# Optimization experiments

Measured on AMD Instinct MI355X. Metric: run time of the kernel, lower is better.

## Reference

```python
import jax, jax.numpy as jnp
import numpy as np

B, K_MAIN, D = 2048, 511, 64


def setup_inputs() -> dict:
    key = jax.random.key(0)
    ks = jax.random.split(key, 8)
    return {
        "vals": jax.random.uniform(ks[0], (B, K_MAIN, D), dtype=jnp.float32),
        "log_density": jax.random.normal(ks[1], (K_MAIN, D), dtype=jnp.float32),
        "logits": jax.random.normal(ks[2], (K_MAIN, D), dtype=jnp.float32),
        "beta_raw": jax.random.normal(ks[3], (K_MAIN,), dtype=jnp.float32),
        "null_vals": jax.random.uniform(ks[4], (B,), dtype=jnp.float32),
        "null_log_density": jax.random.normal(ks[5], (D,), dtype=jnp.float32),
        "null_logits": jax.random.normal(ks[6], (D,), dtype=jnp.float32),
        "null_beta_raw": jax.random.normal(ks[7], (1,), dtype=jnp.float32),
    }


def reference(vals, log_density, logits, beta_raw, null_vals,
              null_log_density, null_logits, null_beta_raw):
    # MenuElement.weights = softmax(logits) per element; beta = clamp(softplus, 0, 10)
    weights = jax.nn.softmax(logits, axis=1)                      # (K_main, D)
    betas = jnp.clip(jax.nn.softplus(beta_raw), 0.0, 10.0)        # (K_main,)
    ld = jnp.clip(log_density, -10.0, 0.0)                        # (K_main, D)
    log_weights = jnp.log(weights + 1e-10) + ld                   # (K_main, D)
    M = jnp.max(log_weights, axis=1, keepdims=True)               # (K_main, 1)
    w_exp = jnp.exp(log_weights - M)                              # (K_main, D)
    # weighted reduction over D for every (valuation b, menu element k)
    weighted_sum = jnp.einsum('bkd,kd->bk', vals, w_exp)          # (B, K_main)
    u_main = jnp.exp(M[:, 0])[None, :] * weighted_sum - betas[None, :]

    # null element
    null_w = jax.nn.softmax(null_logits, axis=0)                  # (D,)
    null_ld = jnp.clip(null_log_density, -10.0, 0.0)
    log_weight_null = jnp.log(null_w + 1e-10) + null_ld           # (D,)
    null_beta = jnp.clip(jax.nn.softplus(null_beta_raw), 0.0, 10.0)[0]
    u_null = jnp.exp(log_weight_null[0]) * null_vals - null_beta  # (B,)

    U = jnp.concatenate([u_main, u_null[:, None]], axis=1)        # (B, K)
    return U
```

## Files before the change

### kernel.cpp

```cpp
#include <hip/hip_runtime.h>
#include <hip/hip_bf16.h>
#include <math.h>

#define B_SZ   2048
#define K_MAIN 511
#define K_OUT  512
#define D_SZ   64

#define WS_COEF  0
#define WS_BETAS (K_MAIN * D_SZ)

typedef float f4v __attribute__((ext_vector_type(4)));

__device__ __forceinline__ float softplus_clip(float x) {
    float sp = (x > 20.f) ? x : log1pf(expf(x));
    return fminf(fmaxf(sp, 0.f), 10.f);
}

__global__ void precompute_kernel(const float* __restrict__ log_density,
                                  const float* __restrict__ logits,
                                  const float* __restrict__ beta_raw,
                                  const float* __restrict__ null_log_density,
                                  const float* __restrict__ null_logits,
                                  const float* __restrict__ null_beta_raw,
                                  const float* __restrict__ null_vals,
                                  float* __restrict__ ws,
                                  float* __restrict__ out) {
    const int k    = blockIdx.x;
    const int lane = threadIdx.x;

    {
        float lg = logits[k * D_SZ + lane];
        float m = lg;
        #pragma unroll
        for (int off = 1; off < 64; off <<= 1) m = fmaxf(m, __shfl_xor(m, off));
        float e = expf(lg - m);
        float s = e;
        #pragma unroll
        for (int off = 1; off < 64; off <<= 1) s += __shfl_xor(s, off);
        float w = e / s;
        float ld = fminf(fmaxf(log_density[k * D_SZ + lane], -10.f), 0.f);
        ws[WS_COEF + k * D_SZ + lane] = (w + 1e-10f) * expf(ld);
        if (lane == 0) {
            ws[WS_BETAS + k] = softplus_clip(beta_raw[k]);
        }
    }

    if (k < (B_SZ / 64)) {
        float lg = null_logits[lane];
        float m = lg;
        #pragma unroll
        for (int off = 1; off < 64; off <<= 1) m = fmaxf(m, __shfl_xor(m, off));
        float e = expf(lg - m);
        float s = e;
        #pragma unroll
        for (int off = 1; off < 64; off <<= 1) s += __shfl_xor(s, off);
        float w0 = expf(null_logits[0] - m) / s;
        float ld0 = fminf(fmaxf(null_log_density[0], -10.f), 0.f);
        float c_null = (w0 + 1e-10f) * expf(ld0);
        float nbeta  = softplus_clip(null_beta_raw[0]);
        const int b = k * 64 + lane;
        out[(size_t)b * K_OUT + K_MAIN] = c_null * null_vals[b] - nbeta;
    }
}

__global__ void __launch_bounds__(256)
main_kernel(const float* __restrict__ vals,
            const float* __restrict__ ws,
            float* __restrict__ out) {
    const float* __restrict__ coef  = ws + WS_COEF;
    const float* __restrict__ betas = ws + WS_BETAS;

    const unsigned tid     = blockIdx.x * blockDim.x + threadIdx.x;
    const unsigned lane    = threadIdx.x & 63u;
    const unsigned wave    = tid >> 6;
    const unsigned nwaves  = (gridDim.x * blockDim.x) >> 6;
    const unsigned sub     = lane >> 4;
    const unsigned d0      = (lane & 15u) << 2;

    const unsigned total_rows = B_SZ * K_MAIN;
    const unsigned nquads     = total_rows >> 4;

    for (unsigned q = wave; q < nquads; q += nwaves) {
        const unsigned r0 = (q << 4) + sub;

        const f4v v0 = *reinterpret_cast<const f4v*>(vals + (size_t)r0 * D_SZ + d0);
        const f4v v1 = *reinterpret_cast<const f4v*>(vals + (size_t)(r0 + 4) * D_SZ + d0);
        const f4v v2 = *reinterpret_cast<const f4v*>(vals + (size_t)(r0 + 8) * D_SZ + d0);
        const f4v v3 = *reinterpret_cast<const f4v*>(vals + (size_t)(r0 + 12) * D_SZ + d0);

        unsigned k0 = r0 % K_MAIN;
        unsigned b0 = r0 / K_MAIN;
        unsigned k1 = k0 + 4, b1 = b0; if (k1 >= K_MAIN) { k1 -= K_MAIN; ++b1; }
        unsigned k2 = k1 + 4, b2 = b1; if (k2 >= K_MAIN) { k2 -= K_MAIN; ++b2; }
        unsigned k3 = k2 + 4, b3 = b2; if (k3 >= K_MAIN) { k3 -= K_MAIN; ++b3; }

        const f4v c0 = *reinterpret_cast<const f4v*>(coef + (size_t)k0 * D_SZ + d0);
        const f4v c1 = *reinterpret_cast<const f4v*>(coef + (size_t)k1 * D_SZ + d0);
        const f4v c2 = *reinterpret_cast<const f4v*>(coef + (size_t)k2 * D_SZ + d0);
        const f4v c3 = *reinterpret_cast<const f4v*>(coef + (size_t)k3 * D_SZ + d0);

        float p0 = v0.x * c0.x + v0.y * c0.y + v0.z * c0.z + v0.w * c0.w;
        float p1 = v1.x * c1.x + v1.y * c1.y + v1.z * c1.z + v1.w * c1.w;
        float p2 = v2.x * c2.x + v2.y * c2.y + v2.z * c2.z + v2.w * c2.w;
        float p3 = v3.x * c3.x + v3.y * c3.y + v3.z * c3.z + v3.w * c3.w;

        p0 += __shfl_xor(p0, 1);  p1 += __shfl_xor(p1, 1);
        p2 += __shfl_xor(p2, 1);  p3 += __shfl_xor(p3, 1);
        p0 += __shfl_xor(p0, 2);  p1 += __shfl_xor(p1, 2);
        p2 += __shfl_xor(p2, 2);  p3 += __shfl_xor(p3, 2);
        p0 += __shfl_xor(p0, 4);  p1 += __shfl_xor(p1, 4);
        p2 += __shfl_xor(p2, 4);  p3 += __shfl_xor(p3, 4);
        p0 += __shfl_xor(p0, 8);  p1 += __shfl_xor(p1, 8);
        p2 += __shfl_xor(p2, 8);  p3 += __shfl_xor(p3, 8);

        if ((lane & 15u) == 0u) {
            out[(size_t)b0 * K_OUT + k0] = p0 - betas[k0];
            out[(size_t)b1 * K_OUT + k1] = p1 - betas[k1];
            out[(size_t)b2 * K_OUT + k2] = p2 - betas[k2];
            out[(size_t)b3 * K_OUT + k3] = p3 - betas[k3];
        }
    }
}

extern "C" void kernel_launch(void* const* d_in, const int* in_sizes, int n_in,
                              void* d_out, int out_size, void* d_ws, size_t ws_size,
                              hipStream_t stream) {
    const float* vals             = (const float*)d_in[0];
    const float* log_density      = (const float*)d_in[1];
    const float* logits           = (const float*)d_in[2];
    const float* beta_raw         = (const float*)d_in[3];
    const float* null_vals        = (const float*)d_in[4];
    const float* null_log_density = (const float*)d_in[5];
    const float* null_logits      = (const float*)d_in[6];
    const float* null_beta_raw    = (const float*)d_in[7];

    float* out = (float*)d_out;
    float* ws  = (float*)d_ws;

    precompute_kernel<<<K_MAIN, 64, 0, stream>>>(log_density, logits, beta_raw,
                                                 null_log_density, null_logits,
                                                 null_beta_raw, null_vals, ws, out);

    main_kernel<<<4096, 256, 0, stream>>>(vals, ws, out);
}
```

Baseline: 48.90 us.

## Fuse precompute and main kernels into one cooperative launch with grid sync

Merges the coefficient/beta precompute kernel and the main dot-product kernel into a single cooperative kernel. Waves first compute coefficients and the null column, then a grid-wide barrier separates that phase from the persistent streaming reduction over vals. This removes one kernel launch and the inter-kernel gap. In exchange it adds a grid sync, caps the grid at 1024 blocks so they can be co-resident, and adds a launch_bounds occupancy hint.

After: 121.1 us. +147.7%, slower.

```diff
diff --git a/kernel.cpp b/kernel.cpp
--- a/kernel.cpp
+++ b/kernel.cpp
@@ -1,6 +1,8 @@
 #include <hip/hip_runtime.h>
-#include <hip/hip_bf16.h>
+#include <hip/hip_cooperative_groups.h>
 #include <math.h>
+
+namespace cg = cooperative_groups;
 
 #define B_SZ   2048
 #define K_MAIN 511
@@ -10,6 +12,8 @@
 #define WS_COEF  0
 #define WS_BETAS (K_MAIN * D_SZ)
 
+#define GRID_BLOCKS 1024
+
 typedef float f4v __attribute__((ext_vector_type(4)));
 
 __device__ __forceinline__ float softplus_clip(float x) {
@@ -17,19 +21,23 @@
     return fminf(fmaxf(sp, 0.f), 10.f);
 }
 
-__global__ void precompute_kernel(const float* __restrict__ log_density,
-                                  const float* __restrict__ logits,
-                                  const float* __restrict__ beta_raw,
-                                  const float* __restrict__ null_log_density,
-                                  const float* __restrict__ null_logits,
-                                  const float* __restrict__ null_beta_raw,
-                                  const float* __restrict__ null_vals,
-                                  float* __restrict__ ws,
-                                  float* __restrict__ out) {
-    const int k    = blockIdx.x;
-    const int lane = threadIdx.x;
+__global__ void __launch_bounds__(256, 4)
+fused_kernel(const float* __restrict__ vals,
+             const float* __restrict__ log_density,
+             const float* __restrict__ logits,
+             const float* __restrict__ beta_raw,
+             const float* __restrict__ null_vals,
+             const float* __restrict__ null_log_density,
+             const float* __restrict__ null_logits,
+             const float* __restrict__ null_beta_raw,
+             float* __restrict__ ws,
+             float* __restrict__ out) {
+    const unsigned tid   = blockIdx.x * blockDim.x + threadIdx.x;
+    const unsigned lane  = threadIdx.x & 63u;
+    const unsigned gwave = tid >> 6;
 
-    {
+    if (gwave < K_MAIN) {
+        const unsigned k = gwave;
         float lg = logits[k * D_SZ + lane];
         float m = lg;
         #pragma unroll
@@ -44,9 +52,7 @@
         if (lane == 0) {
             ws[WS_BETAS + k] = softplus_clip(beta_raw[k]);
         }
-    }
-
-    if (k < (B_SZ / 64)) {
+    } else if (gwave < K_MAIN + B_SZ / 64) {
         float lg = null_logits[lane];
         float m = lg;
         #pragma unroll
@@ -59,29 +65,23 @@
         float ld0 = fminf(fmaxf(null_log_density[0], -10.f), 0.f);
         float c_null = (w0 + 1e-10f) * expf(ld0);
         float nbeta  = softplus_clip(null_beta_raw[0]);
-        const int b = k * 64 + lane;
+        const unsigned b = (gwave - K_MAIN) * 64 + lane;
         out[(size_t)b * K_OUT + K_MAIN] = c_null * null_vals[b] - nbeta;
     }
-}
 
-__global__ void __launch_bounds__(256)
-main_kernel(const float* __restrict__ vals,
-            const float* __restrict__ ws,
-            float* __restrict__ out) {
+    cg::this_grid().sync();
+
     const float* __restrict__ coef  = ws + WS_COEF;
     const float* __restrict__ betas = ws + WS_BETAS;
 
-    const unsigned tid     = blockIdx.x * blockDim.x + threadIdx.x;
-    const unsigned lane    = threadIdx.x & 63u;
-    const unsigned wave    = tid >> 6;
-    const unsigned nwaves  = (gridDim.x * blockDim.x) >> 6;
-    const unsigned sub     = lane >> 4;
-    const unsigned d0      = (lane & 15u) << 2;
+    const unsigned nwaves = (gridDim.x * blockDim.x) >> 6;
+    const unsigned sub    = lane >> 4;
+    const unsigned d0     = (lane & 15u) << 2;
 
     const unsigned total_rows = B_SZ * K_MAIN;
     const unsigned nquads     = total_rows >> 4;
 
-    for (unsigned q = wave; q < nquads; q += nwaves) {
+    for (unsigned q = gwave; q < nquads; q += nwaves) {
         const unsigned r0 = (q << 4) + sub;
 
         const f4v v0 = *reinterpret_cast<const f4v*>(vals + (size_t)r0 * D_SZ + d0);
@@ -138,9 +138,11 @@
     float* out = (float*)d_out;
     float* ws  = (float*)d_ws;
 
-    precompute_kernel<<<K_MAIN, 64, 0, stream>>>(log_density, logits, beta_raw,
-                                                 null_log_density, null_logits,
-                                                 null_beta_raw, null_vals, ws, out);
-
-    main_kernel<<<4096, 256, 0, stream>>>(vals, ws, out);
+    void* args[] = {
+        (void*)&vals, (void*)&log_density, (void*)&logits, (void*)&beta_raw,
+        (void*)&null_vals, (void*)&null_log_density, (void*)&null_logits,
+        (void*)&null_beta_raw, (void*)&ws, (void*)&out,
+    };
+    hipLaunchCooperativeKernel((void*)fused_kernel, dim3(GRID_BLOCKS), dim3(256),
+                               args, 0, stream);
 }
```
